# Kernel optimization log

Hardware: AMD Instinct MI355X
Metric: run time of the kernel (lower is better)

Reference implementation:

```python
import jax, jax.numpy as jnp
import numpy as np
import math

LEVELS = 256
DISTANCES = [1, 3, 5, 7]
ANGLES_DEG = [0, 45, 90, 135]


def _offsets():
    # offset_row = round(sin(theta)*d), offset_col = round(cos(theta)*d)
    offs = []
    for d in DISTANCES:
        row = []
        for theta in ANGLES_DEG:
            rad = theta * math.pi / 180.0
            orow = int(np.round(np.sin(rad) * d))
            ocol = int(np.round(np.cos(rad) * d))
            row.append((orow, ocol))
        offs.append(row)
    return offs


def _glcm_contrast(q, orow, ocol, rows, cols):
    # q: (H, W) int32 quantized image in [0, LEVELS-1]
    sr = 0 if orow > 0 else -orow
    er = rows - orow if orow > 0 else rows
    sc = 0 if ocol > 0 else -ocol
    ec = cols - ocol if ocol > 0 else cols
    a = q[sr:er, sc:ec]
    b = q[sr + orow:er + orow, sc + ocol:ec + ocol]
    idx = (a * LEVELS + b).ravel()
    # scatter-add co-occurrence histogram (the irregular-access core)
    hist = jnp.zeros((LEVELS * LEVELS,), jnp.float32).at[idx].add(1.0)
    P = hist.reshape(LEVELS, LEVELS)
    P = P + P.T                      # symmetric
    s = P.sum()
    P = P / jnp.where(s == 0, 1.0, s)  # normalize
    lv = jnp.arange(LEVELS, dtype=jnp.float32)
    diff2 = (lv[:, None] - lv[None, :]) ** 2
    return (diff2 * P).sum()         # Haralick contrast


def setup_inputs() -> dict:
    key = jax.random.key(0)
    x = jax.random.normal(key, (32, 1, 1024, 1024), dtype=jnp.float32)
    return {"x": x}


def reference(x):
    B, C, H, W = x.shape
    img = x[:, 0]  # (B, H, W), single channel
    # per-image rescale to [0, LEVELS-1] then truncate to int (matches int() cast)
    mn = img.min(axis=(1, 2), keepdims=True)
    mx = img.max(axis=(1, 2), keepdims=True)
    q = ((LEVELS - 1) * (img - mn) / (mx - mn)).astype(jnp.int32)
    q = jax.lax.stop_gradient(q)
    offs = _offsets()
    rows_out = []
    for d_row in offs:
        cols_out = []
        for (orow, ocol) in d_row:
            f = lambda qi, o=orow, c=ocol: _glcm_contrast(qi, o, c, H, W)
            cols_out.append(jax.vmap(f)(q))  # (B,)
        rows_out.append(jnp.stack(cols_out, axis=-1))  # (B, n_angles)
    out = jnp.stack(rows_out, axis=-2)  # (B, n_dist, n_angles)
    return out[:, None, :, :]  # (B, 1, 4, 4)
```

## Files before the change

kernel.cpp:

```cpp
#include <hip/hip_runtime.h>

#define H 1024
#define W 1024
#define NIMG 32
#define NOFF 16
#define NACC 17
#define TH 32
#define TW 256
#define TROWS 39
#define TSTR 304

__device__ __forceinline__ int sdot4i(unsigned a, unsigned b, int c) {
#if __has_builtin(__builtin_amdgcn_sdot4)
    return __builtin_amdgcn_sdot4((int)a, (int)b, c, false);
#else
    c += (int)(signed char)(a)       * (int)(signed char)(b);
    c += (int)(signed char)(a >> 8)  * (int)(signed char)(b >> 8);
    c += (int)(signed char)(a >> 16) * (int)(signed char)(b >> 16);
    c += (int)(signed char)(a >> 24) * (int)(signed char)(b >> 24);
    return c;
#endif
}

__device__ __forceinline__ unsigned funnel(unsigned hi, unsigned lo, int shiftBytes) {
#if __has_builtin(__builtin_amdgcn_alignbit)
    return __builtin_amdgcn_alignbit(hi, lo, shiftBytes * 8);
#else
    unsigned long long pair = (((unsigned long long)hi) << 32) | lo;
    return (unsigned)(pair >> (shiftBytes * 8));
#endif
}

__device__ __forceinline__ int wave_sum(int v) {
    v += __builtin_amdgcn_update_dpp(0, v, 0x111, 0xf, 0xf, false);
    v += __builtin_amdgcn_update_dpp(0, v, 0x112, 0xf, 0xf, false);
    v += __builtin_amdgcn_update_dpp(0, v, 0x114, 0xf, 0xf, false);
    v += __builtin_amdgcn_update_dpp(0, v, 0x118, 0xf, 0xf, false);
    v += __builtin_amdgcn_update_dpp(0, v, 0x142, 0xa, 0xf, false);
    v += __builtin_amdgcn_update_dpp(0, v, 0x143, 0xc, 0xf, false);
    return v;
}

template <int OC>
__device__ __forceinline__ int dot8(const unsigned* w, const unsigned* aw, int acc) {
#pragma unroll
    for (int m = 0; m < 8; ++m) {
        const int S = 16 + 4 * m + OC;
        unsigned b;
        if ((S & 3) == 0) b = w[S >> 2];
        else              b = funnel(w[(S >> 2) + 1], w[S >> 2], S & 3);
        acc = sdot4i(aw[m], b, acc);
    }
    return acc;
}

__device__ __forceinline__ void load16w(const unsigned char* wp, unsigned* w) {
    uint4 t0 = *(const uint4*)(wp);
    uint4 t1 = *(const uint4*)(wp + 16);
    uint4 t2 = *(const uint4*)(wp + 32);
    uint4 t3 = *(const uint4*)(wp + 48);
    w[0] = t0.x;  w[1] = t0.y;  w[2] = t0.z;  w[3] = t0.w;
    w[4] = t1.x;  w[5] = t1.y;  w[6] = t1.z;  w[7] = t1.w;
    w[8] = t2.x;  w[9] = t2.y;  w[10] = t2.z; w[11] = t2.w;
    w[12] = t3.x; w[13] = t3.y; w[14] = t3.z; w[15] = t3.w;
}

__device__ __forceinline__ void load8mid(const unsigned char* wp, unsigned* w) {
    uint4 t1 = *(const uint4*)(wp + 16);
    uint4 t2 = *(const uint4*)(wp + 32);
    w[4] = t1.x;  w[5] = t1.y;  w[6] = t1.z;  w[7] = t1.w;
    w[8] = t2.x;  w[9] = t2.y;  w[10] = t2.z; w[11] = t2.w;
}

__device__ __forceinline__ unsigned pack4(float4 f, float s, float b) {
    unsigned q0 = (unsigned)(int)fmaf(f.x, s, b);
    unsigned q1 = (unsigned)(int)fmaf(f.y, s, b);
    unsigned q2 = (unsigned)(int)fmaf(f.z, s, b);
    unsigned q3 = (unsigned)(int)fmaf(f.w, s, b);
    return (((q0 & 255u)) | ((q1 & 255u) << 8) | ((q2 & 255u) << 16) | ((q3 & 255u) << 24)) ^ 0x80808080u;
}

__global__ __launch_bounds__(256)
void minmax_partial(const float* __restrict__ x, float* __restrict__ pmn,
                    float* __restrict__ pmx, unsigned long long* __restrict__ gacc,
                    int* __restrict__ RowS, int* __restrict__ ColS) {
    int img = blockIdx.y;
    int chunk = blockIdx.x;
    int tid = threadIdx.x;
    if (chunk == 0) {
        if (tid < NACC) gacc[img * NACC + tid] = 0ull;
        if (tid >= 32 && tid < 46) RowS[img * 14 + tid - 32] = 0;
        if (tid >= 64 && tid < 78) ColS[img * 14 + tid - 64] = 0;
    }
    const float4* b4 = (const float4*)(x + (size_t)img * (H * (size_t)W) +
                                       (size_t)chunk * (H * W / 64));
    float mn = INFINITY, mx = -INFINITY;
    for (int i = tid; i < 4096; i += 256) {
        float4 v = b4[i];
        mn = fminf(mn, fminf(fminf(v.x, v.y), fminf(v.z, v.w)));
        mx = fmaxf(mx, fmaxf(fmaxf(v.x, v.y), fmaxf(v.z, v.w)));
    }
    for (int o = 32; o > 0; o >>= 1) {
        mn = fminf(mn, __shfl_down(mn, o, 64));
        mx = fmaxf(mx, __shfl_down(mx, o, 64));
    }
    __shared__ float smn[4], smx[4];
    int wave = tid >> 6, lane = tid & 63;
    if (lane == 0) { smn[wave] = mn; smx[wave] = mx; }
    __syncthreads();
    if (tid == 0) {
        mn = fminf(fminf(smn[0], smn[1]), fminf(smn[2], smn[3]));
        mx = fmaxf(fmaxf(smx[0], smx[1]), fmaxf(smx[2], smx[3]));
        pmn[img * 64 + chunk] = mn;
        pmx[img * 64 + chunk] = mx;
    }
}

__global__ __launch_bounds__(256)
void glcm_main(const float* __restrict__ x, const float* __restrict__ pmn,
               const float* __restrict__ pmx, unsigned long long* __restrict__ gacc,
               int* __restrict__ RowS, int* __restrict__ ColS,
               short* __restrict__ cornerWS) {
    __shared__ __align__(16) unsigned char tile[TROWS * TSTR];
    __shared__ int wsum[4][NACC];
    __shared__ int sRB[7], sCB[7];
    __shared__ float sms[2];
    int tid = threadIdx.x;
    int img = blockIdx.z;
    int gr0 = blockIdx.y * TH;
    int gc0 = blockIdx.x * TW;

    if (tid < 64) {
        float mn = pmn[img * 64 + tid], mx = pmx[img * 64 + tid];
        for (int o = 32; o > 0; o >>= 1) {
            mn = fminf(mn, __shfl_down(mn, o, 64));
            mx = fmaxf(mx, __shfl_down(mx, o, 64));
        }
        if (tid == 0) {
            float sc = 255.0f / (mx - mn);
            sms[0] = sc; sms[1] = -mn * sc;
        }
    }
    if (tid >= 64 && tid < 71) { sRB[tid - 64] = 0; sCB[tid - 64] = 0; }
    __syncthreads();
    float scale = sms[0], nmb = sms[1];
    const float* xi = x + (size_t)img * (H * (size_t)W);

    for (int slot = tid; slot < TROWS * (TSTR / 16); slot += 256) {
        int rr = slot / (TSTR / 16);
        int cc = (slot - rr * (TSTR / 16)) * 16;
        int grow = gr0 + rr;
        int gcol = gc0 - 16 + cc;
        uint4 bytes = make_uint4(0u, 0u, 0u, 0u);
        if (grow < H && gcol >= 0 && gcol < W) {
            const float4* p = (const float4*)(xi + (size_t)grow * W + gcol);
            float4 f0 = p[0], f1 = p[1], f2 = p[2], f3 = p[3];
            bytes.x = pack4(f0, scale, nmb);
            bytes.y = pack4(f1, scale, nmb);
            bytes.z = pack4(f2, scale, nmb);
            bytes.w = pack4(f3, scale, nmb);
        }
        *(uint4*)(tile + rr * TSTR + cc) = bytes;
    }
    __syncthreads();

    int r = tid >> 3;
    int c0 = (tid & 7) * 32;
    const unsigned char* rowp = tile + r * TSTR + 16 + c0;
    const unsigned char* wbase = tile + r * TSTR + c0;

    uint4 av0 = *(const uint4*)(rowp);
    uint4 av1 = *(const uint4*)(rowp + 16);
    unsigned aw[8];
    aw[0] = av0.x; aw[1] = av0.y; aw[2] = av0.z; aw[3] = av0.w;
    aw[4] = av1.x; aw[5] = av1.y; aw[6] = av1.z; aw[7] = av1.w;

    int acc[NACC];
#pragma unroll
    for (int k = 0; k < NACC; ++k) acc[k] = 0;
#pragma unroll
    for (int m = 0; m < 8; ++m) acc[16] = sdot4i(aw[m], aw[m], acc[16]);

    unsigned w[16];
    {
#pragma unroll
        for (int i = 0; i < 8; ++i) w[4 + i] = aw[i];
        uint4 t3 = *(const uint4*)(wbase + 48);
        w[12] = t3.x; w[13] = t3.y; w[14] = t3.z; w[15] = t3.w;
        acc[0]  = dot8<1>(w, aw, acc[0]);
        acc[4]  = dot8<3>(w, aw, acc[4]);
        acc[8]  = dot8<5>(w, aw, acc[8]);
        acc[12] = dot8<7>(w, aw, acc[12]);
    }
    {
        load16w(wbase + 1 * TSTR, w);
        acc[1] = dot8<1>(w, aw, acc[1]);
        acc[2] = dot8<0>(w, aw, acc[2]);
        acc[3] = dot8<-1>(w, aw, acc[3]);
    }
    {
        load16w(wbase + 2 * TSTR, w);
        acc[5] = dot8<2>(w, aw, acc[5]);
        acc[7] = dot8<-2>(w, aw, acc[7]);
    }
    {
        load8mid(wbase + 3 * TSTR, w);
        acc[6] = dot8<0>(w, aw, acc[6]);
    }
    {
        load16w(wbase + 4 * TSTR, w);
        acc[9]  = dot8<4>(w, aw, acc[9]);
        acc[11] = dot8<-4>(w, aw, acc[11]);
    }
    {
        load16w(wbase + 5 * TSTR, w);
        acc[10] = dot8<0>(w, aw, acc[10]);
        acc[13] = dot8<5>(w, aw, acc[13]);
        acc[15] = dot8<-5>(w, aw, acc[15]);
    }
    {
        load8mid(wbase + 7 * TSTR, w);
        acc[14] = dot8<0>(w, aw, acc[14]);
    }

    int wv = tid >> 6, lane = tid & 63;
#pragma unroll
    for (int k = 0; k < NACC; ++k) {
        int t = wave_sum(acc[k]);
        if (lane == 63) wsum[wv][k] = t;
    }

    bool rowTop = (gr0 == 0), rowBot = (gr0 == H - TH);
    bool colLft = (gc0 == 0), colRgt = (gc0 == W - TW);
    if (rowTop || rowBot) {
        int base = rowTop ? 0 : 25;
        for (int idx = tid; idx < 7 * 64; idx += 256) {
            int rr = idx >> 6, ww = idx & 63;
            unsigned v = *(const unsigned*)(tile + (base + rr) * TSTR + 16 + 4 * ww);
            atomicAdd(&sRB[rr], sdot4i(v, v, 0));
        }
    }
    if (colLft || colRgt) {
        int cb = colLft ? 16 : 265;
        if (tid < 7 * TH) {
            int rr = tid / 7, j = tid - rr * 7;
            int s = (int)(signed char)tile[rr * TSTR + cb + j];
            atomicAdd(&sCB[j], s * s);
        }
    }
    if (tid < 49) {
        int i = tid / 7, j = tid - i * 7;
        if (rowTop && colLft) {
            int s = (int)(signed char)tile[i * TSTR + 16 + j];
            cornerWS[(img * 4 + 0) * 49 + tid] = (short)(s * s);
        }
        if (rowTop && colRgt) {
            int s = (int)(signed char)tile[i * TSTR + 271 - j];
            cornerWS[(img * 4 + 1) * 49 + tid] = (short)(s * s);
        }
        if (rowBot && colLft) {
            int s = (int)(signed char)tile[(31 - i) * TSTR + 16 + j];
            cornerWS[(img * 4 + 2) * 49 + tid] = (short)(s * s);
        }
        if (rowBot && colRgt) {
            int s = (int)(signed char)tile[(31 - i) * TSTR + 271 - j];
            cornerWS[(img * 4 + 3) * 49 + tid] = (short)(s * s);
        }
    }
    __syncthreads();
    if (tid < NACC) {
        int s = wsum[0][tid] + wsum[1][tid] + wsum[2][tid] + wsum[3][tid];
        atomicAdd(&gacc[img * NACC + tid], (unsigned long long)(long long)s);
    }
    if (tid < 7) {
        if (rowTop) atomicAdd(&RowS[img * 14 + tid], sRB[tid]);
        if (rowBot) atomicAdd(&RowS[img * 14 + 7 + tid], sRB[tid]);
        if (colLft) atomicAdd(&ColS[img * 14 + tid], sCB[tid]);
        if (colRgt) atomicAdd(&ColS[img * 14 + 7 + tid], sCB[tid]);
    }
}

__global__ __launch_bounds__(512)
void finalize_k(const unsigned long long* __restrict__ gacc,
                const int* __restrict__ RowS, const int* __restrict__ ColS,
                const short* __restrict__ cornerWS, float* __restrict__ out) {
    __shared__ int cps[NIMG][4][8][8];
    int tid = threadIdx.x;
    if (tid < NIMG * 4) {
        int img = tid >> 2, c4 = tid & 3;
        const short* cr = cornerWS + (img * 4 + c4) * 49;
        for (int r = 0; r < 8; ++r)
            for (int c = 0; c < 8; ++c) {
                int v = 0;
                if (r && c)
                    v = cps[img][c4][r - 1][c] + cps[img][c4][r][c - 1]
                      - cps[img][c4][r - 1][c - 1] + (int)cr[(r - 1) * 7 + (c - 1)];
                cps[img][c4][r][c] = v;
            }
    }
    __syncthreads();
    if (tid < NIMG * NOFF) {
        const int ORO[16] = {0,1,1,1, 0,2,3,2, 0,4,5,4, 0,5,7,5};
        const int OCO[16] = {1,1,0,-1, 3,2,0,-2, 5,4,0,-4, 7,5,0,-5};
        int img = tid >> 4, k = tid & 15;
        int orr = ORO[k], oc = OCO[k], aoc = oc < 0 ? -oc : oc;
        long long RT = 0, RB = 0, CL = 0, CR = 0;
        for (int i = 0; i < orr; ++i) { RT += RowS[img * 14 + i]; RB += RowS[img * 14 + 13 - i]; }
        for (int i = 0; i < aoc; ++i) { CL += ColS[img * 14 + i]; CR += ColS[img * 14 + 13 - i]; }
        long long CA = oc > 0 ? CR : CL;
        long long CB = oc > 0 ? CL : CR;
        long long PSa = (oc >= 0) ? cps[img][3][orr][aoc] : cps[img][2][orr][aoc];
        long long PSb = (oc >= 0) ? cps[img][0][orr][aoc] : cps[img][1][orr][aoc];
        long long corr = -(RT + RB + CA + CB) + PSa + PSb;
        long long cross = (long long)gacc[img * NACC + k];
        long long tsum  = (long long)gacc[img * NACC + 16];
        long long num = 2 * tsum + corr - 2 * cross;
        double n = (double)(H - orr) * (double)(W - aoc);
        out[tid] = (float)((double)num / n);
    }
}

extern "C" void kernel_launch(void* const* d_in, const int* in_sizes, int n_in,
                              void* d_out, int out_size, void* d_ws, size_t ws_size,
                              hipStream_t stream) {
    const float* x = (const float*)d_in[0];
    float* out = (float*)d_out;
    char* ws = (char*)d_ws;
    float* pmn = (float*)ws;
    float* pmx = (float*)(ws + 8192);
    unsigned long long* gacc = (unsigned long long*)(ws + 16384);
    int* RowS = (int*)(ws + 20736);
    int* ColS = (int*)(ws + 22528);
    short* cornerWS = (short*)(ws + 24320);

    minmax_partial<<<dim3(64, NIMG), 256, 0, stream>>>(x, pmn, pmx, gacc, RowS, ColS);
    glcm_main<<<dim3(W / TW, H / TH, NIMG), 256, 0, stream>>>(x, pmn, pmx, gacc,
                                                              RowS, ColS, cornerWS);
    finalize_k<<<1, 512, 0, stream>>>(gacc, RowS, ColS, cornerWS, out);
}
```

Before: 229.7 us.

## Double tile height to 64 rows with 512 threads and share funnel shifts

```diff
diff --git a/kernel.cpp b/kernel.cpp
--- a/kernel.cpp
+++ b/kernel.cpp
@@ -5,10 +5,12 @@
 #define NIMG 32
 #define NOFF 16
 #define NACC 17
-#define TH 32
+#define TH 64
 #define TW 256
-#define TROWS 39
+#define TROWS 71
 #define TSTR 304
+#define NTHR 512
+#define NWAVE 8
 
 __device__ __forceinline__ int sdot4i(unsigned a, unsigned b, int c) {
 #if __has_builtin(__builtin_amdgcn_sdot4)
@@ -116,13 +118,13 @@
     }
 }
 
-__global__ __launch_bounds__(256)
+__global__ __launch_bounds__(NTHR)
 void glcm_main(const float* __restrict__ x, const float* __restrict__ pmn,
                const float* __restrict__ pmx, unsigned long long* __restrict__ gacc,
                int* __restrict__ RowS, int* __restrict__ ColS,
-               short* __restrict__ cornerWS) {
+               int* __restrict__ cornerWS) {
     __shared__ __align__(16) unsigned char tile[TROWS * TSTR];
-    __shared__ int wsum[4][NACC];
+    __shared__ int wsum[NWAVE][NACC];
     __shared__ int sRB[7], sCB[7];
     __shared__ float sms[2];
     int tid = threadIdx.x;
@@ -146,7 +148,7 @@
     float scale = sms[0], nmb = sms[1];
     const float* xi = x + (size_t)img * (H * (size_t)W);
 
-    for (int slot = tid; slot < TROWS * (TSTR / 16); slot += 256) {
+    for (int slot = tid; slot < TROWS * (TSTR / 16); slot += NTHR) {
         int rr = slot / (TSTR / 16);
         int cc = (slot - rr * (TSTR / 16)) * 16;
         int grow = gr0 + rr;
@@ -187,10 +189,19 @@
         for (int i = 0; i < 8; ++i) w[4 + i] = aw[i];
         uint4 t3 = *(const uint4*)(wbase + 48);
         w[12] = t3.x; w[13] = t3.y; w[14] = t3.z; w[15] = t3.w;
-        acc[0]  = dot8<1>(w, aw, acc[0]);
-        acc[4]  = dot8<3>(w, aw, acc[4]);
-        acc[8]  = dot8<5>(w, aw, acc[8]);
-        acc[12] = dot8<7>(w, aw, acc[12]);
+        unsigned f1[9], f3[9];
+#pragma unroll
+        for (int k = 0; k < 9; ++k) {
+            f1[k] = funnel(w[5 + k], w[4 + k], 1);
+            f3[k] = funnel(w[5 + k], w[4 + k], 3);
+        }
+#pragma unroll
+        for (int m = 0; m < 8; ++m) {
+            acc[0]  = sdot4i(aw[m], f1[m],     acc[0]);
+            acc[8]  = sdot4i(aw[m], f1[m + 1], acc[8]);
+            acc[4]  = sdot4i(aw[m], f3[m],     acc[4]);
+            acc[12] = sdot4i(aw[m], f3[m + 1], acc[12]);
+        }
     }
     {
         load16w(wbase + 1 * TSTR, w);
@@ -200,8 +211,14 @@
     }
     {
         load16w(wbase + 2 * TSTR, w);
-        acc[5] = dot8<2>(w, aw, acc[5]);
-        acc[7] = dot8<-2>(w, aw, acc[7]);
+        unsigned f2[10];
+#pragma unroll
+        for (int k = 0; k < 10; ++k) f2[k] = funnel(w[4 + k], w[3 + k], 2);
+#pragma unroll
+        for (int m = 0; m < 8; ++m) {
+            acc[5] = sdot4i(aw[m], f2[m + 1], acc[5]);
+            acc[7] = sdot4i(aw[m], f2[m],     acc[7]);
+        }
     }
     {
         load8mid(wbase + 3 * TSTR, w);
@@ -233,8 +250,8 @@
     bool rowTop = (gr0 == 0), rowBot = (gr0 == H - TH);
     bool colLft = (gc0 == 0), colRgt = (gc0 == W - TW);
     if (rowTop || rowBot) {
-        int base = rowTop ? 0 : 25;
-        for (int idx = tid; idx < 7 * 64; idx += 256) {
+        int base = rowTop ? 0 : TH - 7;
+        for (int idx = tid; idx < 7 * 64; idx += NTHR) {
             int rr = idx >> 6, ww = idx & 63;
             unsigned v = *(const unsigned*)(tile + (base + rr) * TSTR + 16 + 4 * ww);
             atomicAdd(&sRB[rr], sdot4i(v, v, 0));
@@ -252,24 +269,26 @@
         int i = tid / 7, j = tid - i * 7;
         if (rowTop && colLft) {
             int s = (int)(signed char)tile[i * TSTR + 16 + j];
-            cornerWS[(img * 4 + 0) * 49 + tid] = (short)(s * s);
+            cornerWS[(img * 4 + 0) * 49 + tid] = s * s;
         }
         if (rowTop && colRgt) {
             int s = (int)(signed char)tile[i * TSTR + 271 - j];
-            cornerWS[(img * 4 + 1) * 49 + tid] = (short)(s * s);
+            cornerWS[(img * 4 + 1) * 49 + tid] = s * s;
         }
         if (rowBot && colLft) {
-            int s = (int)(signed char)tile[(31 - i) * TSTR + 16 + j];
-            cornerWS[(img * 4 + 2) * 49 + tid] = (short)(s * s);
+            int s = (int)(signed char)tile[(TH - 1 - i) * TSTR + 16 + j];
+            cornerWS[(img * 4 + 2) * 49 + tid] = s * s;
         }
         if (rowBot && colRgt) {
-            int s = (int)(signed char)tile[(31 - i) * TSTR + 271 - j];
-            cornerWS[(img * 4 + 3) * 49 + tid] = (short)(s * s);
+            int s = (int)(signed char)tile[(TH - 1 - i) * TSTR + 271 - j];
+            cornerWS[(img * 4 + 3) * 49 + tid] = s * s;
         }
     }
     __syncthreads();
     if (tid < NACC) {
-        int s = wsum[0][tid] + wsum[1][tid] + wsum[2][tid] + wsum[3][tid];
+        int s = 0;
+#pragma unroll
+        for (int w8 = 0; w8 < NWAVE; ++w8) s += wsum[w8][tid];
         atomicAdd(&gacc[img * NACC + tid], (unsigned long long)(long long)s);
     }
     if (tid < 7) {
@@ -283,20 +302,25 @@
 __global__ __launch_bounds__(512)
 void finalize_k(const unsigned long long* __restrict__ gacc,
                 const int* __restrict__ RowS, const int* __restrict__ ColS,
-                const short* __restrict__ cornerWS, float* __restrict__ out) {
+                const int* __restrict__ cornerWS, float* __restrict__ out) {
     __shared__ int cps[NIMG][4][8][8];
     int tid = threadIdx.x;
     if (tid < NIMG * 4) {
         int img = tid >> 2, c4 = tid & 3;
-        const short* cr = cornerWS + (img * 4 + c4) * 49;
-        for (int r = 0; r < 8; ++r)
-            for (int c = 0; c < 8; ++c) {
-                int v = 0;
-                if (r && c)
-                    v = cps[img][c4][r - 1][c] + cps[img][c4][r][c - 1]
-                      - cps[img][c4][r - 1][c - 1] + (int)cr[(r - 1) * 7 + (c - 1)];
-                cps[img][c4][r][c] = v;
-            }
+        const int* cr = cornerWS + tid * 49;
+        int prev[8];
+#pragma unroll
+        for (int c = 0; c < 8; ++c) { prev[c] = 0; cps[img][c4][0][c] = 0; }
+#pragma unroll
+        for (int rr = 1; rr < 8; ++rr) {
+            int cur[8];
+            cur[0] = 0;
+#pragma unroll
+            for (int c = 1; c < 8; ++c)
+                cur[c] = prev[c] + cur[c - 1] - prev[c - 1] + cr[(rr - 1) * 7 + (c - 1)];
+#pragma unroll
+            for (int c = 0; c < 8; ++c) { cps[img][c4][rr][c] = cur[c]; prev[c] = cur[c]; }
+        }
     }
     __syncthreads();
     if (tid < NIMG * NOFF) {
@@ -331,10 +355,10 @@
     unsigned long long* gacc = (unsigned long long*)(ws + 16384);
     int* RowS = (int*)(ws + 20736);
     int* ColS = (int*)(ws + 22528);
-    short* cornerWS = (short*)(ws + 24320);
+    int* cornerWS = (int*)(ws + 24320);
 
     minmax_partial<<<dim3(64, NIMG), 256, 0, stream>>>(x, pmn, pmx, gacc, RowS, ColS);
-    glcm_main<<<dim3(W / TW, H / TH, NIMG), 256, 0, stream>>>(x, pmn, pmx, gacc,
-                                                              RowS, ColS, cornerWS);
+    glcm_main<<<dim3(W / TW, H / TH, NIMG), NTHR, 0, stream>>>(x, pmn, pmx, gacc,
+                                                               RowS, ColS, cornerWS);
     finalize_k<<<1, 512, 0, stream>>>(gacc, RowS, ColS, cornerWS, out);
 }
```

Result: slower. 234.6 us (+2.1%).
